# Performance work log

Measured on AMD Instinct MI355X. Metric: run time of the kernel, lower is better.

Reference implementation:

```python
import jax, jax.numpy as jnp
import numpy as np

BOS = 1  # TOKENS['BOS'] assumed


def gru_scan(x_seq, h0, W_ih, W_hh, b_ih, b_hh):
    """PyTorch-style single-layer GRU over time. x_seq: (T,B,H), h0: (B,H)."""
    def step(h, x):
        gi = x @ W_ih.T + b_ih          # (B,3H)
        gh = h @ W_hh.T + b_hh          # (B,3H)
        i_r, i_z, i_n = jnp.split(gi, 3, axis=-1)
        h_r, h_z, h_n = jnp.split(gh, 3, axis=-1)
        r = jax.nn.sigmoid(i_r + h_r)
        z = jax.nn.sigmoid(i_z + h_z)
        n = jnp.tanh(i_n + r * h_n)
        h_new = (1.0 - z) * n + z * h
        return h_new, h_new
    hT, outs = jax.lax.scan(step, h0, x_seq)
    return outs, hT


def setup_inputs() -> dict:
    key = jax.random.key(0)
    ks = jax.random.split(key, 24)
    H = 256
    V = 50003       # user_size + 3
    TAGV = 966
    T_in, T_tgt, T_tag, B = 50, 40, 20, 32
    s = 0.02
    inp = {
        'input_tensor': jax.random.randint(ks[0], (T_in, B), 0, V),
        'target_tensor': jax.random.randint(ks[1], (T_tgt, B), 0, V),
        'tag_tensor': jax.random.randint(ks[2], (T_tag, B), 0, TAGV),
        'enc_emb': jax.random.normal(ks[3], (V, H), jnp.float32) * s,
        'enc_Wih': jax.random.normal(ks[4], (3 * H, H), jnp.float32) * s,
        'enc_Whh': jax.random.normal(ks[5], (3 * H, H), jnp.float32) * s,
        'enc_bih': jax.random.normal(ks[6], (3 * H,), jnp.float32) * s,
        'enc_bhh': jax.random.normal(ks[7], (3 * H,), jnp.float32) * s,
        'tag_emb': jax.random.normal(ks[8], (TAGV, H), jnp.float32) * s,
        'tag_Wih': jax.random.normal(ks[9], (3 * H, H), jnp.float32) * s,
        'tag_Whh': jax.random.normal(ks[10], (3 * H, H), jnp.float32) * s,
        'tag_bih': jax.random.normal(ks[11], (3 * H,), jnp.float32) * s,
        'tag_bhh': jax.random.normal(ks[12], (3 * H,), jnp.float32) * s,
        'proj_W': jax.random.normal(ks[13], (H, 2 * H), jnp.float32) * s,
        'proj_b': jax.random.normal(ks[14], (H,), jnp.float32) * s,
        'dec_Wih': jax.random.normal(ks[15], (3 * H, H), jnp.float32) * s,
        'dec_Whh': jax.random.normal(ks[16], (3 * H, H), jnp.float32) * s,
        'dec_bih': jax.random.normal(ks[17], (3 * H,), jnp.float32) * s,
        'dec_bhh': jax.random.normal(ks[18], (3 * H,), jnp.float32) * s,
        'out_W': jax.random.normal(ks[19], (V, H), jnp.float32) * s,
        'out_b': jax.random.normal(ks[20], (V,), jnp.float32) * s,
    }
    return inp


def reference(input_tensor, target_tensor, tag_tensor,
              enc_emb, enc_Wih, enc_Whh, enc_bih, enc_bhh,
              tag_emb, tag_Wih, tag_Whh, tag_bih, tag_bhh,
              proj_W, proj_b,
              dec_Wih, dec_Whh, dec_bih, dec_bhh,
              out_W, out_b):
    T_in, B = input_tensor.shape
    T_tgt = target_tensor.shape[0]
    H = enc_emb.shape[1]
    h0 = jnp.zeros((B, H), enc_emb.dtype)

    # encoder over input tokens
    _, enc_h = gru_scan(enc_emb[input_tensor], h0, enc_Wih, enc_Whh, enc_bih, enc_bhh)
    # tag encoder
    _, tag_h = gru_scan(tag_emb[tag_tensor], h0, tag_Wih, tag_Whh, tag_bih, tag_bhh)

    # proj(cat(tag_hidden, encoder_hidden)); dropout = identity (eval)
    merged = jnp.concatenate([tag_h, enc_h], axis=-1) @ proj_W.T + proj_b  # (B,H)

    # teacher forcing: decoder inputs = [BOS, target[:-1]]
    dec_in = jnp.concatenate(
        [jnp.full((1, B), BOS, dtype=target_tensor.dtype), target_tensor[:-1]], axis=0)
    dec_x = jax.nn.relu(enc_emb[dec_in])                 # (T_tgt,B,H), shared embedding
    dec_outs, _ = gru_scan(dec_x, merged, dec_Wih, dec_Whh, dec_bih, dec_bhh)
    logits = dec_outs @ out_W.T + out_b                  # (T_tgt,B,V)

    # criterion = CrossEntropyLoss(mean over batch), summed over timesteps
    logp = jax.nn.log_softmax(logits, axis=-1)
    nll = -jnp.take_along_axis(logp, target_tensor[..., None], axis=-1)[..., 0]  # (T_tgt,B)
    decoder_loss = nll.mean(axis=1).sum()
    avg_loss = decoder_loss / T_tgt
    decoder_outputs = logits[:, None, :, :]              # (T_tgt,1,B,V) like torch.stack of unsqueezed
    return (decoder_loss, avg_loss, decoder_outputs)
```

## Files before the change

### kernel.cpp

```cpp
#include <hip/hip_runtime.h>
#include <hip/hip_bf16.h>
#include <math.h>


#define H 256
#define H3 768
#define NBATCH 32
#define TIN 50
#define TTGT 40
#define TTAG 20
#define VSZ 50003
#define VP 50048
#define NT 782
#define MT 1280
#define NGI 330
#define NCVT 12512

typedef float f32x4 __attribute__((ext_vector_type(4)));
typedef short short8 __attribute__((ext_vector_type(8)));

__device__ __forceinline__ float dot4(float4 a, float4 b) {
    return a.x * b.x + a.y * b.y + a.z * b.z + a.w * b.w;
}

__device__ __forceinline__ float bf2f(short s) {
    unsigned int u = ((unsigned int)(unsigned short)s) << 16;
    return __builtin_bit_cast(float, u);
}

__device__ __forceinline__ void bar_lgkm() {
    asm volatile("s_waitcnt lgkmcnt(0)" ::: "memory");
    __builtin_amdgcn_s_barrier();
    __builtin_amdgcn_sched_barrier(0);
}

__global__ void k_prep(const float* eWih, const float* tWih, const float* dWih,
                       const float* projW, const float* eWhh, const float* tWhh,
                       const float* dWhh, float* d0, float* d1, float* d2,
                       float* d3, __hip_bfloat16* p0, __hip_bfloat16* p1,
                       __hip_bfloat16* p2) {
    int which = blockIdx.y;
    if (which < 4) {
        const float* s;
        float* d;
        int N, K;
        switch (which) {
            case 0: s = eWih; d = d0; N = H3; K = H; break;
            case 1: s = tWih; d = d1; N = H3; K = H; break;
            case 2: s = dWih; d = d2; N = H3; K = H; break;
            default: s = projW; d = d3; N = H; K = 2 * H; break;
        }
        int n = blockIdx.x;
        if (n >= N) return;
        for (int k = threadIdx.x; k < K; k += 256)
            d[(size_t)(k >> 2) * (N * 4) + n * 4 + (k & 3)] = s[(size_t)n * K + k];
    } else {
        if (blockIdx.x >= 96) return;
        const float* s = which == 4 ? eWhh : (which == 5 ? tWhh : dWhh);
        __hip_bfloat16* d = which == 4 ? p0 : (which == 5 ? p1 : p2);
        int idx = blockIdx.x * 256 + threadIdx.x;
        int lane = idx & 63;
        int f = (idx >> 6) % 24;
        int w = idx / (24 * 64);
        int ks = f / 3, q = f % 3;
        int row = (q << 8) + (w << 4) + (lane & 15);
        int k = (ks << 5) + ((lane >> 4) << 3);
#pragma unroll
        for (int j = 0; j < 8; ++j)
            d[(size_t)idx * 8 + j] = __float2bfloat16(s[(size_t)row * H + k + j]);
    }
}

__global__ __launch_bounds__(256) void k_gi_cvt(
    const int* in_toks, const int* tag_toks, const int* tgt_toks,
    const float* enc_emb, const float* tag_emb, const float* W4e,
    const float* W4t, const float* W4d, const float* bih_e, const float* bhh_e,
    const float* bih_t, const float* bhh_t, const float* bih_d,
    const float* bhh_d, __hip_bfloat16* gi_e, __hip_bfloat16* gi_t,
    __hip_bfloat16* gi_d, const float* outW, __hip_bfloat16* outWb) {
    int bx = blockIdx.x, tid = threadIdx.x;
    if (bx >= NGI) {
        int i4 = ((bx - NGI) * 256 + tid) * 4;
        if (i4 >= VP * H) return;
        int row = i4 >> 8;
        float4 v;
        if (row < VSZ) v = *(const float4*)(outW + i4);
        else v = make_float4(0.f, 0.f, 0.f, 0.f);
        outWb[i4 + 0] = __float2bfloat16(v.x);
        outWb[i4 + 1] = __float2bfloat16(v.y);
        outWb[i4 + 2] = __float2bfloat16(v.z);
        outWb[i4 + 3] = __float2bfloat16(v.w);
        return;
    }
    __shared__ float x[NBATCH][H];
    int g = bx % 3, tt = bx / 3;
    const int* toks;
    const float* emb;
    const float* W4;
    const float* bihp;
    const float* bhhp;
    __hip_bfloat16* gip;
    int t, mode;
    if (tt < TIN) {
        toks = in_toks; emb = enc_emb; W4 = W4e; bihp = bih_e; bhhp = bhh_e;
        gip = gi_e; t = tt; mode = 0;
    } else if (tt < TIN + TTAG) {
        toks = tag_toks; emb = tag_emb; W4 = W4t; bihp = bih_t; bhhp = bhh_t;
        gip = gi_t; t = tt - TIN; mode = 0;
    } else {
        toks = tgt_toks; emb = enc_emb; W4 = W4d; bihp = bih_d; bhhp = bhh_d;
        gip = gi_d; t = tt - TIN - TTAG; mode = 2;
    }
    for (int b = 0; b < NBATCH; ++b) {
        int tok;
        if (mode == 2) tok = (t == 0) ? 1 : toks[(t - 1) * NBATCH + b];
        else tok = toks[t * NBATCH + b];
        float v = emb[(size_t)tok * H + tid];
        if (mode == 2) v = fmaxf(v, 0.0f);
        x[b][tid] = v;
    }
    __syncthreads();
    int nb_ = tid & 63, mg = tid >> 6;
    float acc[4][8];
#pragma unroll
    for (int j = 0; j < 4; ++j)
#pragma unroll
        for (int mi = 0; mi < 8; ++mi) acc[j][mi] = 0.f;
    for (int k4 = 0; k4 < 64; ++k4) {
        const float4* wrow = (const float4*)(W4 + (size_t)k4 * 3072);
        float4 w0 = wrow[g * 256 + nb_];
        float4 w1 = wrow[g * 256 + nb_ + 64];
        float4 w2 = wrow[g * 256 + nb_ + 128];
        float4 w3 = wrow[g * 256 + nb_ + 192];
#pragma unroll
        for (int mi = 0; mi < 8; ++mi) {
            float4 xv = *(const float4*)&x[mg * 8 + mi][k4 * 4];
            acc[0][mi] += dot4(xv, w0);
            acc[1][mi] += dot4(xv, w1);
            acc[2][mi] += dot4(xv, w2);
            acc[3][mi] += dot4(xv, w3);
        }
    }
#pragma unroll
    for (int j = 0; j < 4; ++j) {
        int n = g * 256 + nb_ + j * 64;
        float bv = bihp[n] + (g < 2 ? bhhp[n] : 0.0f);
        int nn = n & 255;
        int ww = nn >> 4, lrr = nn & 15;
#pragma unroll
        for (int mi = 0; mi < 8; ++mi) {
            int bm = mg * 8 + mi;
            int locb = bm >> 4, lmm = bm & 15;
            int lgg = lmm >> 2, reg = lmm & 3;
            size_t idx = ((size_t)(t * 2 + locb) * 16 + ww) * 1024 +
                         reg * 256 + (lgg * 16 + lrr) * 4 + g;
            gip[idx] = __float2bfloat16(acc[j][mi] + bv);
        }
    }
}

__global__ __launch_bounds__(1024) void k_scan(
    int nset1,
    const __hip_bfloat16* gi1, const __hip_bfloat16* W1, const float* bhh1,
    const float* h01, float* hT1, __hip_bfloat16* out1, int T1,
    const __hip_bfloat16* gi2, const __hip_bfloat16* W2, const float* bhh2,
    const float* h02, float* hT2, __hip_bfloat16* out2, int T2) {
    __shared__ uint4 WL[16 * 6 * 64];
    __shared__ uint4 HBF[2][512];

    int blk = blockIdx.x, tid = threadIdx.x;
    const __hip_bfloat16 *gip, *Wg;
    const float *bhh, *h0;
    float* hTp;
    __hip_bfloat16* outp;
    int T, loc;
    if (blk < nset1) {
        gip = gi1; Wg = W1; bhh = bhh1; h0 = h01; hTp = hT1; outp = out1;
        T = T1; loc = blk;
    } else {
        gip = gi2; Wg = W2; bhh = bhh2; h0 = h02; hTp = hT2; outp = out2;
        T = T2; loc = blk - nset1;
    }
    int mb = loc * 16;
    int w = tid >> 6, lane = tid & 63, lr = lane & 15, lg = lane >> 4;

    short8 wreg[18];
    const uint4* Wg4 = (const uint4*)Wg;
#pragma unroll
    for (int f = 0; f < 18; ++f) {
        uint4 v = Wg4[(size_t)(w * 24 + f) * 64 + lane];
        wreg[f] = *(short8*)&v;
    }
#pragma unroll
    for (int i = 0; i < 6; ++i)
        WL[(w * 6 + i) * 64 + lane] = Wg4[(size_t)(w * 24 + 18 + i) * 64 + lane];

    float bnv = bhh[512 + w * 16 + lr];

    float hprev[4];
    short* HB16 = (short*)HBF;
#pragma unroll
    for (int reg = 0; reg < 4; ++reg) {
        int row = lg * 4 + reg, col = w * 16 + lr;
        float hv = h0 ? h0[(size_t)(mb + row) * H + col] : 0.0f;
        hprev[reg] = hv;
        __hip_bfloat16 q = __float2bfloat16(hv);
        int ch = w * 2 + (lr >> 3);
        int slot = ch ^ (row & 7);
        HB16[row * 256 + slot * 8 + (lr & 7)] = *(short*)&q;
    }
    uint2 gv[4];
    {
        const __hip_bfloat16* gp = gip + ((size_t)loc * 16 + w) * 1024;
#pragma unroll
        for (int reg = 0; reg < 4; ++reg)
            gv[reg] = *(const uint2*)(gp + reg * 256 + lane * 4);
    }
    __syncthreads();

    const short8* HSbase = (const short8*)HBF;
    const short8* WLs = (const short8*)WL;
    for (int t = 0; t < T; ++t) {
        int p = t & 1, p2 = p ^ 1;
        const short8* HS = HSbase + p * 512;
        f32x4 acc[3];
        acc[0] = (f32x4){0.f, 0.f, 0.f, 0.f};
        acc[1] = acc[0];
        acc[2] = (f32x4){bnv, bnv, bnv, bnv};
#pragma unroll
        for (int ks = 0; ks < 6; ++ks) {
            short8 a = HS[lr * 32 + ((ks * 4 + lg) ^ (lr & 7))];
#pragma unroll
            for (int q = 0; q < 3; ++q)
                acc[q] = __builtin_amdgcn_mfma_f32_16x16x32_bf16(
                    a, wreg[ks * 3 + q], acc[q], 0, 0, 0);
        }
#pragma unroll
        for (int ks = 6; ks < 8; ++ks) {
            short8 a = HS[lr * 32 + ((ks * 4 + lg) ^ (lr & 7))];
#pragma unroll
            for (int q = 0; q < 3; ++q) {
                short8 bv = WLs[(w * 6 + (ks - 6) * 3 + q) * 64 + lane];
                acc[q] = __builtin_amdgcn_mfma_f32_16x16x32_bf16(
                    a, bv, acc[q], 0, 0, 0);
            }
        }
#pragma unroll
        for (int reg = 0; reg < 4; ++reg) {
            uint2 u = gv[reg];
            float gr = bf2f((short)(u.x & 0xffff));
            float gz = bf2f((short)(u.x >> 16));
            float gn = bf2f((short)(u.y & 0xffff));
            float er = __expf(-(gr + acc[0][reg]));
            float r = __builtin_amdgcn_rcpf(1.0f + er);
            float ez = __expf(-(gz + acc[1][reg]));
            float z = __builtin_amdgcn_rcpf(1.0f + ez);
            float xx = gn + r * acc[2][reg];
            float e2 = __expf(-2.0f * fabsf(xx));
            float nv = copysignf((1.0f - e2) * __builtin_amdgcn_rcpf(1.0f + e2), xx);
            float hnew = (1.0f - z) * nv + z * hprev[reg];
            hprev[reg] = hnew;
            __hip_bfloat16 qb = __float2bfloat16(hnew);
            int row = lg * 4 + reg;
            int ch = w * 2 + (lr >> 3);
            int slot = ch ^ (row & 7);
            HB16[p2 * 4096 + row * 256 + slot * 8 + (lr & 7)] = *(short*)&qb;
        }
        if (t + 1 < T) {
            const __hip_bfloat16* gp =
                gip + ((size_t)((t + 1) * 2 + loc) * 16 + w) * 1024;
#pragma unroll
            for (int reg = 0; reg < 4; ++reg)
                gv[reg] = *(const uint2*)(gp + reg * 256 + lane * 4);
        }
        if (outp && t >= 1 && tid < 512) {
            int lb = tid >> 5, ch2 = tid & 31;
            short8 hv = HSbase[p * 512 + lb * 32 + (ch2 ^ (lb & 7))];
            *(short8*)(outp + (size_t)((t - 1) * NBATCH + mb + lb) * H + ch2 * 8) = hv;
        }
        bar_lgkm();
    }
    if (outp && tid < 512) {
        int lb = tid >> 5, ch2 = tid & 31;
        short8 hv = HSbase[(T & 1) * 512 + lb * 32 + (ch2 ^ (lb & 7))];
        *(short8*)(outp + (size_t)((T - 1) * NBATCH + mb + lb) * H + ch2 * 8) = hv;
    }
    if (hTp) {
#pragma unroll
        for (int reg = 0; reg < 4; ++reg) {
            int row = lg * 4 + reg, col = w * 16 + lr;
            hTp[(size_t)(mb + row) * H + col] = hprev[reg];
        }
    }
}

__global__ void k_proj(const float* tag_h, const float* enc_h,
                       const float* W4p, const float* pb, float* merged) {
    __shared__ float c[2 * H];
    int b = blockIdx.x, tid = threadIdx.x;
    c[tid] = tag_h[b * H + tid];
    c[H + tid] = enc_h[b * H + tid];
    __syncthreads();
    float acc = 0.f;
#pragma unroll 4
    for (int k4 = 0; k4 < 128; ++k4) {
        float4 cv = *(const float4*)&c[k4 * 4];
        float4 wv = ((const float4*)(W4p + (size_t)k4 * 1024))[tid];
        acc += dot4(cv, wv);
    }
    merged[b * H + tid] = acc + pb[tid];
}

__global__ __launch_bounds__(256) void k_logits(const __hip_bfloat16* A,
                                                const __hip_bfloat16* Bw,
                                                const float* bias, float* dout,
                                                float* pmax, float* psum) {
    __shared__ uint4 bsm[2048];
    __shared__ float cst[4][16][68];
    int bid = blockIdx.x;
    int wg = (bid & 7) * 1955 + (bid >> 3);
    int nblk = wg / 20, mblk = wg % 20;
    int m0 = mblk * 64, n0 = nblk * 64;
    int tid = threadIdx.x;
    int wave = tid >> 6, lane = tid & 63, lr = lane & 15, lg = lane >> 4;
    const uint4* Bg = (const uint4*)(Bw + (size_t)n0 * H);
#pragma unroll
    for (int i = 0; i < 8; ++i) {
        int c = tid + i * 256;
        int r = c >> 5, g = c & 31;
        bsm[(r << 5) | (g ^ (r & 7))] = Bg[c];
    }
    short8 areg[8];
    const uint4* Ar = (const uint4*)(A + (size_t)(m0 + wave * 16 + lr) * H);
#pragma unroll
    for (int ks = 0; ks < 8; ++ks) {
        uint4 v = Ar[ks * 4 + lg];
        areg[ks] = *(short8*)&v;
    }
    float biasv[4];
    bool valid[4];
#pragma unroll
    for (int ns = 0; ns < 4; ++ns) {
        int n = n0 + ns * 16 + lr;
        valid[ns] = (n < VSZ);
        biasv[ns] = valid[ns] ? bias[n] : 0.f;
    }
    __syncthreads();
    f32x4 acc[4];
#pragma unroll
    for (int ns = 0; ns < 4; ++ns) acc[ns] = (f32x4){0.f, 0.f, 0.f, 0.f};
    const short8* L = (const short8*)bsm;
#pragma unroll
    for (int ks = 0; ks < 8; ++ks) {
        int ga = ks * 4 + lg;
#pragma unroll
        for (int ns = 0; ns < 4; ++ns) {
            int rb = ns * 16 + lr;
            acc[ns] = __builtin_amdgcn_mfma_f32_16x16x32_bf16(
                areg[ks], L[(rb << 5) | (ga ^ (rb & 7))], acc[ns], 0, 0, 0);
        }
    }
    float* cw = &cst[wave][0][0];
#pragma unroll
    for (int reg = 0; reg < 4; ++reg) {
        int m = m0 + wave * 16 + lg * 4 + reg;
        float v[4];
        float rm = -INFINITY;
#pragma unroll
        for (int ns = 0; ns < 4; ++ns) {
            v[ns] = acc[ns][reg] + biasv[ns];
            if (valid[ns]) rm = fmaxf(rm, v[ns]);
            cw[(lg * 4 + reg) * 68 + ns * 16 + lr] = v[ns];
        }
        for (int off = 1; off < 16; off <<= 1) rm = fmaxf(rm, __shfl_xor(rm, off));
        float se = 0.f;
#pragma unroll
        for (int ns = 0; ns < 4; ++ns)
            if (valid[ns]) se += __expf(v[ns] - rm);
        for (int off = 1; off < 16; off <<= 1) se += __shfl_xor(se, off);
        if (lr == 0) {
            pmax[(size_t)m * NT + nblk] = rm;
            psum[(size_t)m * NT + nblk] = se;
        }
    }
    float* dbase = dout + 2 + (size_t)(m0 + wave * 16) * VSZ + n0;
    bool colok = (n0 + lane < VSZ);
#pragma unroll
    for (int rl = 0; rl < 16; ++rl) {
        float val = cst[wave][rl][lane];
        if (colok)
            __builtin_nontemporal_store(val, &dbase[(size_t)rl * VSZ + lane]);
    }
}

__global__ void k_lse(const float* pmax, const float* psum, float* lse) {
    int m = blockIdx.x, tid = threadIdx.x;
    __shared__ float sm[4];
    float lm = -INFINITY;
    for (int i = tid; i < NT; i += 256) lm = fmaxf(lm, pmax[(size_t)m * NT + i]);
    for (int off = 1; off < 64; off <<= 1) lm = fmaxf(lm, __shfl_xor(lm, off));
    if ((tid & 63) == 0) sm[tid >> 6] = lm;
    __syncthreads();
    float M = fmaxf(fmaxf(sm[0], sm[1]), fmaxf(sm[2], sm[3]));
    __syncthreads();
    float s = 0.f;
    for (int i = tid; i < NT; i += 256)
        s += psum[(size_t)m * NT + i] * __expf(pmax[(size_t)m * NT + i] - M);
    for (int off = 1; off < 64; off <<= 1) s += __shfl_xor(s, off);
    if ((tid & 63) == 0) sm[tid >> 6] = s;
    __syncthreads();
    if (tid == 0) lse[m] = M + logf(sm[0] + sm[1] + sm[2] + sm[3]);
}

__global__ void k_loss(const float* lse, const int* tgt, float* dout) {
    int tid = threadIdx.x;
    __shared__ float sm[4];
    float s = 0.f;
    for (int m = tid; m < MT; m += 256) {
        int tg = tgt[m];
        s += lse[m] - dout[2 + (size_t)m * VSZ + tg];
    }
    for (int off = 1; off < 64; off <<= 1) s += __shfl_xor(s, off);
    if ((tid & 63) == 0) sm[tid >> 6] = s;
    __syncthreads();
    if (tid == 0) {
        float total = sm[0] + sm[1] + sm[2] + sm[3];
        dout[0] = total / 32.0f;
        dout[1] = total / 1280.0f;
    }
}

extern "C" void kernel_launch(void* const* d_in, const int* in_sizes, int n_in,
                              void* d_out, int out_size, void* d_ws,
                              size_t ws_size, hipStream_t stream) {
    const int* input_tensor = (const int*)d_in[0];
    const int* target_tensor = (const int*)d_in[1];
    const int* tag_tensor = (const int*)d_in[2];
    const float* enc_emb = (const float*)d_in[3];
    const float* enc_Wih = (const float*)d_in[4];
    const float* enc_Whh = (const float*)d_in[5];
    const float* enc_bih = (const float*)d_in[6];
    const float* enc_bhh = (const float*)d_in[7];
    const float* tag_emb = (const float*)d_in[8];
    const float* tag_Wih = (const float*)d_in[9];
    const float* tag_Whh = (const float*)d_in[10];
    const float* tag_bih = (const float*)d_in[11];
    const float* tag_bhh = (const float*)d_in[12];
    const float* proj_W = (const float*)d_in[13];
    const float* proj_b = (const float*)d_in[14];
    const float* dec_Wih = (const float*)d_in[15];
    const float* dec_Whh = (const float*)d_in[16];
    const float* dec_bih = (const float*)d_in[17];
    const float* dec_bhh = (const float*)d_in[18];
    const float* out_W = (const float*)d_in[19];
    const float* out_b = (const float*)d_in[20];

    char* wsb = (char*)d_ws;
    size_t o = 0;
    auto alloc = [&](size_t bytes) {
        size_t r = o;
        o += (bytes + 511) & ~(size_t)511;
        return r;
    };
    float* W4_enc_ih = (float*)(wsb + alloc(H3 * H * 4));
    float* W4_tag_ih = (float*)(wsb + alloc(H3 * H * 4));
    float* W4_dec_ih = (float*)(wsb + alloc(H3 * H * 4));
    float* W4_proj   = (float*)(wsb + alloc(H * 2 * H * 4));
    __hip_bfloat16* gi_enc = (__hip_bfloat16*)(wsb + alloc((size_t)TIN * 65536));
    __hip_bfloat16* gi_tag = (__hip_bfloat16*)(wsb + alloc((size_t)TTAG * 65536));
    __hip_bfloat16* gi_dec = (__hip_bfloat16*)(wsb + alloc((size_t)TTGT * 65536));
    float* enc_h  = (float*)(wsb + alloc(NBATCH * H * 4));
    float* tag_h  = (float*)(wsb + alloc(NBATCH * H * 4));
    float* merged = (float*)(wsb + alloc(NBATCH * H * 4));
    float* lse    = (float*)(wsb + alloc(MT * 4));
    __hip_bfloat16* Wp_enc = (__hip_bfloat16*)(wsb + alloc(H3 * H * 2));
    __hip_bfloat16* Wp_tag = (__hip_bfloat16*)(wsb + alloc(H3 * H * 2));
    __hip_bfloat16* Wp_dec = (__hip_bfloat16*)(wsb + alloc(H3 * H * 2));
    __hip_bfloat16* outWb  = (__hip_bfloat16*)(wsb + alloc((size_t)VP * H * 2));
    __hip_bfloat16* decA   = (__hip_bfloat16*)(wsb + alloc((size_t)MT * H * 2));
    float* pmax = (float*)(wsb + alloc((size_t)MT * NT * 4));
    float* psum = (float*)(wsb + alloc((size_t)MT * NT * 4));

    float* dout = (float*)d_out;

    k_prep<<<dim3(H3, 7), 256, 0, stream>>>(
        enc_Wih, tag_Wih, dec_Wih, proj_W, enc_Whh, tag_Whh, dec_Whh,
        W4_enc_ih, W4_tag_ih, W4_dec_ih, W4_proj, Wp_enc, Wp_tag, Wp_dec);

    k_gi_cvt<<<NGI + NCVT, 256, 0, stream>>>(
        input_tensor, tag_tensor, target_tensor, enc_emb, tag_emb, W4_enc_ih,
        W4_tag_ih, W4_dec_ih, enc_bih, enc_bhh, tag_bih, tag_bhh, dec_bih,
        dec_bhh, gi_enc, gi_tag, gi_dec, out_W, outWb);

    k_scan<<<4, 1024, 0, stream>>>(
        2, gi_enc, Wp_enc, enc_bhh, nullptr, enc_h, nullptr, TIN,
        gi_tag, Wp_tag, tag_bhh, nullptr, tag_h, nullptr, TTAG);

    k_proj<<<NBATCH, 256, 0, stream>>>(tag_h, enc_h, W4_proj, proj_b, merged);

    k_scan<<<2, 1024, 0, stream>>>(
        2, gi_dec, Wp_dec, dec_bhh, merged, nullptr, decA, TTGT,
        nullptr, nullptr, nullptr, nullptr, nullptr, nullptr, 0);

    k_logits<<<NT * 20, 256, 0, stream>>>(decA, outWb, out_b, dout, pmax, psum);

    k_lse<<<MT, 256, 0, stream>>>(pmax, psum, lse);

    k_loss<<<1, 256, 0, stream>>>(lse, target_tensor, dout);
}
```

Measured before the change: 448.0 us.

## Fuse projection into decoder scan and widen logits blocks to share B tile

Removes the separate k_proj launch by computing the merged hidden state inside the decoder k_scan prologue, using the weight LDS region as scratch before the weights are loaded. k_logits now uses 512-thread blocks covering two M tiles per N tile, so each B tile staged in LDS is reused twice and half as many blocks are launched, with the XCD-aware block remapping adjusted to match. A small unroll pragma is also added to the embedding gather loop. The fused projection runs serially on only 2 blocks and adds LDS pressure and extra barriers to the scan's startup.

```diff
diff --git a/kernel.cpp b/kernel.cpp
--- a/kernel.cpp
+++ b/kernel.cpp
@@ -111,6 +111,7 @@
         toks = tgt_toks; emb = enc_emb; W4 = W4d; bihp = bih_d; bhhp = bhh_d;
         gip = gi_d; t = tt - TIN - TTAG; mode = 2;
     }
+#pragma unroll 4
     for (int b = 0; b < NBATCH; ++b) {
         int tok;
         if (mode == 2) tok = (t == 0) ? 1 : toks[(t - 1) * NBATCH + b];
@@ -164,7 +165,8 @@
     const __hip_bfloat16* gi1, const __hip_bfloat16* W1, const float* bhh1,
     const float* h01, float* hT1, __hip_bfloat16* out1, int T1,
     const __hip_bfloat16* gi2, const __hip_bfloat16* W2, const float* bhh2,
-    const float* h02, float* hT2, __hip_bfloat16* out2, int T2) {
+    const float* h02, float* hT2, __hip_bfloat16* out2, int T2,
+    const float* tagh, const float* ench, const float* W4p, const float* pb) {
     __shared__ uint4 WL[16 * 6 * 64];
     __shared__ uint4 HBF[2][512];
 
@@ -184,31 +186,71 @@
     int mb = loc * 16;
     int w = tid >> 6, lane = tid & 63, lr = lane & 15, lg = lane >> 4;
 
-    short8 wreg[18];
-    const uint4* Wg4 = (const uint4*)Wg;
-#pragma unroll
-    for (int f = 0; f < 18; ++f) {
-        uint4 v = Wg4[(size_t)(w * 24 + f) * 64 + lane];
-        wreg[f] = *(short8*)&v;
-    }
-#pragma unroll
-    for (int i = 0; i < 6; ++i)
-        WL[(w * 6 + i) * 64 + lane] = Wg4[(size_t)(w * 24 + 18 + i) * 64 + lane];
-
-    float bnv = bhh[512 + w * 16 + lr];
+    float* CC = (float*)WL;
+    float* MM = ((float*)WL) + 8192;
+    if (W4p) {
+#pragma unroll
+        for (int i = 0; i < 8; ++i) {
+            int idx = i * 1024 + tid;
+            int row = idx >> 9, col = idx & 511;
+            float v = (col < 256)
+                          ? tagh[(size_t)(mb + row) * H + col]
+                          : ench[(size_t)(mb + row) * H + (col - 256)];
+            CC[idx] = v;
+        }
+        __syncthreads();
+        {
+            int col = tid & 255, rg = tid >> 8;
+            float a0 = 0.f, a1 = 0.f, a2 = 0.f, a3 = 0.f;
+            for (int k4 = 0; k4 < 128; ++k4) {
+                float4 wv = ((const float4*)(W4p + (size_t)k4 * 1024))[col];
+                float4 c0 = *(const float4*)&CC[(rg * 4 + 0) * 512 + k4 * 4];
+                float4 c1 = *(const float4*)&CC[(rg * 4 + 1) * 512 + k4 * 4];
+                float4 c2 = *(const float4*)&CC[(rg * 4 + 2) * 512 + k4 * 4];
+                float4 c3 = *(const float4*)&CC[(rg * 4 + 3) * 512 + k4 * 4];
+                a0 += dot4(c0, wv);
+                a1 += dot4(c1, wv);
+                a2 += dot4(c2, wv);
+                a3 += dot4(c3, wv);
+            }
+            float bv = pb[col];
+            MM[(rg * 4 + 0) * 256 + col] = a0 + bv;
+            MM[(rg * 4 + 1) * 256 + col] = a1 + bv;
+            MM[(rg * 4 + 2) * 256 + col] = a2 + bv;
+            MM[(rg * 4 + 3) * 256 + col] = a3 + bv;
+        }
+        __syncthreads();
+    }
 
     float hprev[4];
     short* HB16 = (short*)HBF;
 #pragma unroll
     for (int reg = 0; reg < 4; ++reg) {
         int row = lg * 4 + reg, col = w * 16 + lr;
-        float hv = h0 ? h0[(size_t)(mb + row) * H + col] : 0.0f;
+        float hv;
+        if (W4p) hv = MM[row * 256 + col];
+        else hv = h0 ? h0[(size_t)(mb + row) * H + col] : 0.0f;
         hprev[reg] = hv;
         __hip_bfloat16 q = __float2bfloat16(hv);
         int ch = w * 2 + (lr >> 3);
         int slot = ch ^ (row & 7);
         HB16[row * 256 + slot * 8 + (lr & 7)] = *(short*)&q;
     }
+    __syncthreads();
+
+    short8 wreg[18];
+    const uint4* Wg4 = (const uint4*)Wg;
+#pragma unroll
+    for (int f = 0; f < 18; ++f) {
+        uint4 v = Wg4[(size_t)(w * 24 + f) * 64 + lane];
+        wreg[f] = *(short8*)&v;
+    }
+#pragma unroll
+    for (int i = 0; i < 6; ++i)
+        WL[(w * 6 + i) * 64 + lane] = Wg4[(size_t)(w * 24 + 18 + i) * 64 + lane];
+
+    float bnv = bhh[512 + w * 16 + lr];
+
     uint2 gv[4];
     {
         const __hip_bfloat16* gp = gip + ((size_t)loc * 16 + w) * 1024;
@@ -294,44 +336,31 @@
     }
 }
 
-__global__ void k_proj(const float* tag_h, const float* enc_h,
-                       const float* W4p, const float* pb, float* merged) {
-    __shared__ float c[2 * H];
-    int b = blockIdx.x, tid = threadIdx.x;
-    c[tid] = tag_h[b * H + tid];
-    c[H + tid] = enc_h[b * H + tid];
-    __syncthreads();
-    float acc = 0.f;
-#pragma unroll 4
-    for (int k4 = 0; k4 < 128; ++k4) {
-        float4 cv = *(const float4*)&c[k4 * 4];
-        float4 wv = ((const float4*)(W4p + (size_t)k4 * 1024))[tid];
-        acc += dot4(cv, wv);
-    }
-    merged[b * H + tid] = acc + pb[tid];
-}
-
-__global__ __launch_bounds__(256) void k_logits(const __hip_bfloat16* A,
+__global__ __launch_bounds__(512) void k_logits(const __hip_bfloat16* A,
                                                 const __hip_bfloat16* Bw,
                                                 const float* bias, float* dout,
                                                 float* pmax, float* psum) {
     __shared__ uint4 bsm[2048];
-    __shared__ float cst[4][16][68];
+    __shared__ float cst[8][16][68];
     int bid = blockIdx.x;
-    int wg = (bid & 7) * 1955 + (bid >> 3);
-    int nblk = wg / 20, mblk = wg % 20;
-    int m0 = mblk * 64, n0 = nblk * 64;
+    int xcd = bid & 7, off = bid >> 3;
+    int wg = (xcd < 4 ? xcd * 978 : 3912 + (xcd - 4) * 977) + off;
+    int nblk = wg / 10, mpair = wg % 10;
     int tid = threadIdx.x;
     int wave = tid >> 6, lane = tid & 63, lr = lane & 15, lg = lane >> 4;
+    int wg2 = wave >> 2, wsub = wave & 3;
+    int mblk = mpair * 2 + wg2;
+    int m0 = mblk * 64, n0 = nblk * 64;
+
     const uint4* Bg = (const uint4*)(Bw + (size_t)n0 * H);
 #pragma unroll
-    for (int i = 0; i < 8; ++i) {
-        int c = tid + i * 256;
+    for (int i = 0; i < 4; ++i) {
+        int c = tid + i * 512;
         int r = c >> 5, g = c & 31;
         bsm[(r << 5) | (g ^ (r & 7))] = Bg[c];
     }
     short8 areg[8];
-    const uint4* Ar = (const uint4*)(A + (size_t)(m0 + wave * 16 + lr) * H);
+    const uint4* Ar = (const uint4*)(A + (size_t)(m0 + wsub * 16 + lr) * H);
 #pragma unroll
     for (int ks = 0; ks < 8; ++ks) {
         uint4 v = Ar[ks * 4 + lg];
@@ -363,7 +392,7 @@
     float* cw = &cst[wave][0][0];
 #pragma unroll
     for (int reg = 0; reg < 4; ++reg) {
-        int m = m0 + wave * 16 + lg * 4 + reg;
+        int m = m0 + wsub * 16 + lg * 4 + reg;
         float v[4];
         float rm = -INFINITY;
 #pragma unroll
@@ -372,18 +401,18 @@
             if (valid[ns]) rm = fmaxf(rm, v[ns]);
             cw[(lg * 4 + reg) * 68 + ns * 16 + lr] = v[ns];
         }
-        for (int off = 1; off < 16; off <<= 1) rm = fmaxf(rm, __shfl_xor(rm, off));
+        for (int off2 = 1; off2 < 16; off2 <<= 1) rm = fmaxf(rm, __shfl_xor(rm, off2));
         float se = 0.f;
 #pragma unroll
         for (int ns = 0; ns < 4; ++ns)
             if (valid[ns]) se += __expf(v[ns] - rm);
-        for (int off = 1; off < 16; off <<= 1) se += __shfl_xor(se, off);
+        for (int off2 = 1; off2 < 16; off2 <<= 1) se += __shfl_xor(se, off2);
         if (lr == 0) {
             pmax[(size_t)m * NT + nblk] = rm;
             psum[(size_t)m * NT + nblk] = se;
         }
     }
-    float* dbase = dout + 2 + (size_t)(m0 + wave * 16) * VSZ + n0;
+    float* dbase = dout + 2 + (size_t)(m0 + wsub * 16) * VSZ + n0;
     bool colok = (n0 + lane < VSZ);
 #pragma unroll
     for (int rl = 0; rl < 16; ++rl) {
@@ -471,7 +500,6 @@
     __hip_bfloat16* gi_dec = (__hip_bfloat16*)(wsb + alloc((size_t)TTGT * 65536));
     float* enc_h  = (float*)(wsb + alloc(NBATCH * H * 4));
     float* tag_h  = (float*)(wsb + alloc(NBATCH * H * 4));
-    float* merged = (float*)(wsb + alloc(NBATCH * H * 4));
     float* lse    = (float*)(wsb + alloc(MT * 4));
     __hip_bfloat16* Wp_enc = (__hip_bfloat16*)(wsb + alloc(H3 * H * 2));
     __hip_bfloat16* Wp_tag = (__hip_bfloat16*)(wsb + alloc(H3 * H * 2));
@@ -494,15 +522,15 @@
 
     k_scan<<<4, 1024, 0, stream>>>(
         2, gi_enc, Wp_enc, enc_bhh, nullptr, enc_h, nullptr, TIN,
-        gi_tag, Wp_tag, tag_bhh, nullptr, tag_h, nullptr, TTAG);
-
-    k_proj<<<NBATCH, 256, 0, stream>>>(tag_h, enc_h, W4_proj, proj_b, merged);
+        gi_tag, Wp_tag, tag_bhh, nullptr, tag_h, nullptr, TTAG,
+        nullptr, nullptr, nullptr, nullptr);
 
     k_scan<<<2, 1024, 0, stream>>>(
-        2, gi_dec, Wp_dec, dec_bhh, merged, nullptr, decA, TTGT,
-        nullptr, nullptr, nullptr, nullptr, nullptr, nullptr, 0);
-
-    k_logits<<<NT * 20, 256, 0, stream>>>(decA, outWb, out_b, dout, pmax, psum);
+        2, gi_dec, Wp_dec, dec_bhh, nullptr, nullptr, decA, TTGT,
+        nullptr, nullptr, nullptr, nullptr, nullptr, nullptr, 0,
+        tag_h, enc_h, W4_proj, proj_b);
+
+    k_logits<<<NT * 10, 512, 0, stream>>>(decA, outWb, out_b, dout, pmax, psum);
 
     k_lse<<<MT, 256, 0, stream>>>(pmax, psum, lse);
 
```

Result: slower. 462.5 us (+3.2%).
